# Kernel optimization log

Hardware: AMD Instinct MI355X
Metric: run time of the kernel (lower is better)

The kernel has to match this reference:

```python
import jax, jax.numpy as jnp
import numpy as np

B, L, D = 2, 1024, 512          # batch, seq_len, d_model
H, DK, DV, P = 8, 64, 64, 4     # heads, d_k, d_v, num masks
TEMP = DK ** 0.5
EPS = 1e-6


def setup_inputs() -> dict:
    key = jax.random.key(0)
    ks = jax.random.split(key, 11)
    s = 0.04  # ~xavier scale for these fan sizes
    q = jax.random.normal(ks[0], (B, L, D), jnp.float32)
    k = jax.random.normal(ks[1], (B, L, D), jnp.float32)
    v = jax.random.normal(ks[2], (B, L, D), jnp.float32)
    mask = (jax.random.uniform(ks[3], (P, 1, 1, L, L)) > 0.2).astype(jnp.float32)
    w_q = jax.random.normal(ks[4], (H * DK, D), jnp.float32) * s
    w_k = jax.random.normal(ks[5], (H * DK, D), jnp.float32) * s
    w_v = jax.random.normal(ks[6], (H * DV, D), jnp.float32) * s
    fc_w = jax.random.normal(ks[7], (D, H * DV), jnp.float32) * s
    fc_b = jnp.zeros((D,), jnp.float32)
    ln_g = jnp.ones((D,), jnp.float32)
    ln_b = jnp.zeros((D,), jnp.float32)
    return {"q": q, "k": k, "v": v, "mask": mask, "w_q": w_q, "w_k": w_k,
            "w_v": w_v, "fc_w": fc_w, "fc_b": fc_b, "ln_g": ln_g, "ln_b": ln_b}


def reference(q, k, v, mask, w_q, w_k, w_v, fc_w, fc_b, ln_g, ln_b):
    b, lq = q.shape[0], q.shape[1]
    lk = k.shape[1]
    residual = q
    # pre-LayerNorm on q (normalize_before=True)
    mu = jnp.mean(q, axis=-1, keepdims=True)
    var = jnp.mean(jnp.square(q - mu), axis=-1, keepdims=True)
    qn = (q - mu) * jax.lax.rsqrt(var + EPS) * ln_g + ln_b
    # projections -> [B,H,L,dk/dv]
    qh = jnp.einsum('bld,ed->ble', qn, w_q).reshape(b, lq, H, DK).transpose(0, 2, 1, 3)
    kh = jnp.einsum('bld,ed->ble', k, w_k).reshape(b, lk, H, DK).transpose(0, 2, 1, 3)
    vh = jnp.einsum('bld,ed->ble', v, w_v).reshape(b, lk, H, DV).transpose(0, 2, 1, 3)
    # shared scores, computed once: [B,H,Lq,Lk]
    attn = jnp.einsum('bhqd,bhkd->bhqk', qh / TEMP, kh)
    # per-mask additive bias, vectorized over P (dropout is identity in eval)
    ext = (1.0 - mask) * -10000.0                      # [P,1,1,Lq,Lk]
    probs = jax.nn.softmax(attn[None] + ext, axis=-1)  # [P,B,H,Lq,Lk]
    out = jnp.einsum('pbhqk,bhkd->pbhqd', probs, vh)   # [P,B,H,Lq,DV]
    out = out.transpose(0, 1, 3, 2, 4).reshape(P, b, lq, H * DV)
    out = jnp.einsum('pble,de->pbld', out, fc_w) + fc_b
    out = out + residual[None]
    return (out, attn)
```

## Files before the change

kernel.cpp:

```cpp
#include <hip/hip_runtime.h>
#include <math.h>

namespace {

constexpr int B = 2, L = 1024, D = 512, H = 8, DK = 64, DV = 64, P = 4;
constexpr float EPS = 1e-6f;
constexpr float ESHIFT = 16.0f;

typedef float f32x4 __attribute__((ext_vector_type(4)));
typedef short s16x8 __attribute__((ext_vector_type(8)));

__device__ inline unsigned short f2bf(float x) {
  union { float f; unsigned u; } v; v.f = x;
  unsigned r = v.u + 0x7fffu + ((v.u >> 16) & 1u);
  return (unsigned short)(r >> 16);
}

struct Cvt6 {
  const float* s[6];
  unsigned short* d[6];
  int cum[7];
};
constexpr int LNB = B * L;
constexpr int CVB = 3072;
constexpr int MKB = 512;

__global__ __launch_bounds__(256) void prep_kernel(
    const float* __restrict__ x, const float* __restrict__ g,
    const float* __restrict__ bta, unsigned short* __restrict__ y, Cvt6 a,
    const float* __restrict__ mask, unsigned* __restrict__ mpk) {
  int bid = blockIdx.x, t = threadIdx.x;
  if (bid < LNB) {
    const float* xr = x + (size_t)bid * D;
    unsigned short* yr = y + (size_t)bid * D;
    float v0 = xr[t], v1 = xr[t + 256];
    float s = v0 + v1;
#pragma unroll
    for (int off = 32; off; off >>= 1) s += __shfl_down(s, off, 64);
    __shared__ float red[4];
    if ((t & 63) == 0) red[t >> 6] = s;
    __syncthreads();
    float mu = (red[0] + red[1] + red[2] + red[3]) * (1.0f / D);
    float d0 = v0 - mu, d1 = v1 - mu;
    float vs = d0 * d0 + d1 * d1;
#pragma unroll
    for (int off = 32; off; off >>= 1) vs += __shfl_down(vs, off, 64);
    __syncthreads();
    if ((t & 63) == 0) red[t >> 6] = vs;
    __syncthreads();
    float var = (red[0] + red[1] + red[2] + red[3]) * (1.0f / D);
    float rstd = rsqrtf(var + EPS);
    yr[t] = f2bf(d0 * rstd * g[t] + bta[t]);
    yr[t + 256] = f2bf(d1 * rstd * g[t + 256] + bta[t + 256]);
  } else if (bid < LNB + CVB) {
    int e4 = ((bid - LNB) * 256 + t) * 4;
    int ti = 0;
    while (e4 >= a.cum[ti + 1]) ++ti;
    int off = e4 - a.cum[ti];
    float4 v = *(const float4*)(a.s[ti] + off);
    ushort4 o;
    o.x = f2bf(v.x); o.y = f2bf(v.y); o.z = f2bf(v.z); o.w = f2bf(v.w);
    *(ushort4*)(a.d[ti] + off) = o;
  } else {
    int gid = (bid - LNB - CVB) * 256 + t;
    const float4* src = (const float4*)mask + (size_t)gid * 8;
    unsigned bits = 0;
#pragma unroll
    for (int j = 0; j < 8; ++j) {
      float4 vv = src[j];
      bits |= (vv.x != 0.0f ? 1u : 0u) << (j * 4);
      bits |= (vv.y != 0.0f ? 2u : 0u) << (j * 4);
      bits |= (vv.z != 0.0f ? 4u : 0u) << (j * 4);
      bits |= (vv.w != 0.0f ? 8u : 0u) << (j * 4);
    }
    mpk[gid] = bits;
  }
}

template <bool BF16OUT, bool VTOUT>
__global__ __launch_bounds__(256) void bgemm_nt(
    const unsigned short* __restrict__ A, int lda, long sA0, long sA1,
    const unsigned short* __restrict__ Bm, int ldb, long sB0, long sB1,
    void* __restrict__ Cv, int ldc, long sC0, long sC1,
    int Z0, int K, float alpha,
    const float* __restrict__ bias, const float* __restrict__ resid, int rm,
    unsigned short* __restrict__ vtout) {
  int z = blockIdx.z;
  int z0 = z % Z0, z1 = z / Z0;
  A += (size_t)z0 * sA0 + (size_t)z1 * sA1;
  Bm += (size_t)z0 * sB0 + (size_t)z1 * sB1;
  size_t cOff = (size_t)z0 * sC0 + (size_t)z1 * sC1;
  int m0 = blockIdx.y * 128, n0 = blockIdx.x * 128;
  int t = threadIdx.x;
  int w = t >> 6, lane = t & 63, q4 = lane >> 4, ln16 = lane & 15;
  int wm = (w >> 1) * 64, wn = (w & 1) * 64;
  __shared__ __align__(16) unsigned short As[2][128][40];
  __shared__ __align__(16) unsigned short Bs[2][128][40];
  f32x4 acc[4][4];
#pragma unroll
  for (int i = 0; i < 4; ++i)
#pragma unroll
    for (int j = 0; j < 4; ++j)
#pragma unroll
      for (int r = 0; r < 4; ++r) acc[i][j][r] = 0.0f;
  int c0 = t, c1 = t + 256;
  const unsigned short* Ar0 = A + (size_t)(m0 + (c0 >> 2)) * lda + (c0 & 3) * 8;
  const unsigned short* Ar1 = A + (size_t)(m0 + (c1 >> 2)) * lda + (c1 & 3) * 8;
  const unsigned short* Br0 = Bm + (size_t)(n0 + (c0 >> 2)) * ldb + (c0 & 3) * 8;
  const unsigned short* Br1 = Bm + (size_t)(n0 + (c1 >> 2)) * ldb + (c1 & 3) * 8;
  {
    float4 a0 = *(const float4*)Ar0;
    float4 a1 = *(const float4*)Ar1;
    float4 b0 = *(const float4*)Br0;
    float4 b1 = *(const float4*)Br1;
    *(float4*)&As[0][c0 >> 2][(c0 & 3) * 8] = a0;
    *(float4*)&As[0][c1 >> 2][(c1 & 3) * 8] = a1;
    *(float4*)&Bs[0][c0 >> 2][(c0 & 3) * 8] = b0;
    *(float4*)&Bs[0][c1 >> 2][(c1 & 3) * 8] = b1;
  }
  int nIt = K >> 5;
  for (int it = 0; it < nIt; ++it) {
    int cur = it & 1;
    float4 na0, na1, nb0, nb1;
    if (it + 1 < nIt) {
      int kt = (it + 1) * 32;
      na0 = *(const float4*)(Ar0 + kt);
      na1 = *(const float4*)(Ar1 + kt);
      nb0 = *(const float4*)(Br0 + kt);
      nb1 = *(const float4*)(Br1 + kt);
    }
    __syncthreads();
    s16x8 af[4], bf[4];
#pragma unroll
    for (int mi = 0; mi < 4; ++mi)
      af[mi] = *(const s16x8*)&As[cur][wm + mi * 16 + ln16][q4 * 8];
#pragma unroll
    for (int ni = 0; ni < 4; ++ni)
      bf[ni] = *(const s16x8*)&Bs[cur][wn + ni * 16 + ln16][q4 * 8];
#pragma unroll
    for (int mi = 0; mi < 4; ++mi)
#pragma unroll
      for (int ni = 0; ni < 4; ++ni)
        acc[mi][ni] = __builtin_amdgcn_mfma_f32_16x16x32_bf16(
            af[mi], bf[ni], acc[mi][ni], 0, 0, 0);
    if (it + 1 < nIt) {
      int nb = 1 - cur;
      *(float4*)&As[nb][c0 >> 2][(c0 & 3) * 8] = na0;
      *(float4*)&As[nb][c1 >> 2][(c1 & 3) * 8] = na1;
      *(float4*)&Bs[nb][c0 >> 2][(c0 & 3) * 8] = nb0;
      *(float4*)&Bs[nb][c1 >> 2][(c1 & 3) * 8] = nb1;
    }
  }
  if (VTOUT && z0 == 2) {
#pragma unroll
    for (int mi = 0; mi < 4; ++mi)
#pragma unroll
      for (int ni = 0; ni < 4; ++ni) {
        int row0 = m0 + wm + mi * 16 + q4 * 4;
        int col = n0 + wn + ni * 16 + ln16;
        int bb = row0 >> 10, hh = col >> 6, dv = col & 63;
        ushort4 o;
        o.x = f2bf(acc[mi][ni][0]);
        o.y = f2bf(acc[mi][ni][1]);
        o.z = f2bf(acc[mi][ni][2]);
        o.w = f2bf(acc[mi][ni][3]);
        *(ushort4*)&vtout[((size_t)((bb * 8 + hh) * 64 + dv)) * 1024 +
                          (row0 & 1023)] = o;
      }
    return;
  }
#pragma unroll
  for (int mi = 0; mi < 4; ++mi)
#pragma unroll
    for (int r = 0; r < 4; ++r) {
      int row = m0 + wm + mi * 16 + q4 * 4 + r;
#pragma unroll
      for (int ni = 0; ni < 4; ++ni) {
        int col = n0 + wn + ni * 16 + ln16;
        float v = acc[mi][ni][r] * alpha;
        if (bias) v += bias[col];
        if (resid) v += resid[(size_t)(row & rm) * ldc + col];
        if (BF16OUT)
          ((unsigned short*)Cv)[cOff + (size_t)row * ldc + col] = f2bf(v);
        else
          ((float*)Cv)[cOff + (size_t)row * ldc + col] = v;
      }
    }
}

__global__ __launch_bounds__(256, 2) void fattn2_kernel(
    const unsigned short* __restrict__ qh,
    const unsigned short* __restrict__ khm, const unsigned* __restrict__ mpk,
    const unsigned short* __restrict__ vt, float* __restrict__ attn,
    unsigned short* __restrict__ outh) {
  int q0 = blockIdx.x * 32, bh = blockIdx.y;
  int b = bh >> 3, h = bh & 7;
  __shared__ __align__(16) unsigned short Es[3][32][72];
  __shared__ __align__(16) unsigned short Vs[2][64][72];
  __shared__ __align__(16) unsigned short Qs[32][72];
  __shared__ unsigned Mb[2][4][32][2];
  int t = threadIdx.x;
  int w = t >> 6, lane = t & 63, q4 = lane >> 4, ln16 = lane & 15;
  int vr = t >> 2, vk = (t & 3) * 16;
  int mp = t >> 6, mq = (t >> 1) & 31, md = t & 1;
  const unsigned short* vsrc = vt + ((size_t)bh * 64 + vr) * 1024 + vk;
  const unsigned* msrc = mpk + ((size_t)mp * L + q0 + mq) * 32 + md;
  const unsigned short* kbase = khm + (size_t)(b * L) * 512 + h * 64;
  float* arow = attn + (size_t)bh * L * L + (size_t)q0 * L;

  s16x8 ones;
#pragma unroll
  for (int j = 0; j < 8; ++j) ones[j] = (short)0x3F80;
  f32x4 acc[2][4], accs[2];
#pragma unroll
  for (int i = 0; i < 2; ++i) {
#pragma unroll
    for (int r = 0; r < 4; ++r) accs[i][r] = 0.0f;
#pragma unroll
    for (int j = 0; j < 4; ++j)
#pragma unroll
      for (int r = 0; r < 4; ++r) acc[i][j][r] = 0.0f;
  }
  s16x8 kreg[4][2];

#define KLOAD(dd)                                                              \
  do {                                                                         \
    const unsigned short* kb_ =                                                \
        kbase + (size_t)((dd) * 64 + ln16) * 512 + q4 * 8;                     \
    _Pragma("unroll") for (int ni = 0; ni < 4; ++ni)                           \
        _Pragma("unroll") for (int kk = 0; kk < 2; ++kk)                       \
            kreg[ni][kk] = *(const s16x8*)(kb_ + (size_t)ni * 16 * 512 +       \
                                           kk * 32);                           \
  } while (0)

#define QKCHUNK(dd)                                                            \
  do {                                                                         \
    f32x4 a2[2][4];                                                            \
    _Pragma("unroll") for (int mi = 0; mi < 2; ++mi)                           \
        _Pragma("unroll") for (int ni = 0; ni < 4; ++ni)                       \
            _Pragma("unroll") for (int r = 0; r < 4; ++r) a2[mi][ni][r] = 0.f; \
    _Pragma("unroll") for (int kk = 0; kk < 2; ++kk) {                         \
      s16x8 qf[2];                                                             \
      _Pragma("unroll") for (int mi = 0; mi < 2; ++mi) qf[mi] =                \
          *(const s16x8*)&Qs[mi * 16 + ln16][kk * 32 + q4 * 8];                \
      _Pragma("unroll") for (int mi = 0; mi < 2; ++mi)                         \
          _Pragma("unroll") for (int ni = 0; ni < 4; ++ni)                     \
              a2[mi][ni] = __builtin_amdgcn_mfma_f32_16x16x32_bf16(            \
                  qf[mi], kreg[ni][kk], a2[mi][ni], 0, 0, 0);                  \
    }                                                                          \
    int kc_ = (dd) * 64, eb_ = (dd) % 3;                                       \
    _Pragma("unroll") for (int mi = 0; mi < 2; ++mi)                           \
        _Pragma("unroll") for (int r = 0; r < 4; ++r) {                        \
      int row_ = mi * 16 + q4 * 4 + r;                                         \
      _Pragma("unroll") for (int ni = 0; ni < 4; ++ni) {                       \
        int col_ = ni * 16 + ln16;                                             \
        float v_ = a2[mi][ni][r] * 0.125f;                                     \
        arow[(size_t)row_ * L + kc_ + col_] = v_;                              \
        Es[eb_][row_][col_] = f2bf(__expf(v_ - ESHIFT));                       \
      }                                                                        \
    }                                                                          \
  } while (0)

  {
    int qr = t >> 3, qk = (t & 7) * 8;
    *(int4*)&Qs[qr][qk] =
        *(const int4*)(qh + (size_t)(b * L + q0 + qr) * 512 + h * 64 + qk);
  }
  *(int4*)&Vs[0][vr][vk] = *(const int4*)vsrc;
  *(int4*)&Vs[0][vr][vk + 8] = *(const int4*)(vsrc + 8);
  Mb[0][mp][mq][md] = msrc[0];
  KLOAD(w);
  __syncthreads();
  if (w == 0) QKCHUNK(0);
  else if (w == 1) QKCHUNK(1);
  __syncthreads();

  for (int c = 0; c < 16; ++c) {
    int4 nv0, nv1;
    unsigned nmb;
    if (c < 15) {
      const unsigned short* vs = vsrc + (c + 1) * 64;
      nv0 = *(const int4*)vs;
      nv1 = *(const int4*)(vs + 8);
      nmb = msrc[(c + 1) * 2];
    }
    if (c + 4 <= 15 && ((c + 4) & 3) == w) KLOAD(c + 4);
    {
      int b3 = c % 3, bv = c & 1;
      unsigned mby[2][2];
#pragma unroll
      for (int mi = 0; mi < 2; ++mi) {
        unsigned d0 = Mb[bv][w][mi * 16 + ln16][0];
        unsigned d1 = Mb[bv][w][mi * 16 + ln16][1];
        mby[mi][0] = (d0 >> (q4 * 8)) & 0xFFu;
        mby[mi][1] = (d1 >> (q4 * 8)) & 0xFFu;
      }
      s16x8 bfv[4][2];
#pragma unroll
      for (int ni = 0; ni < 4; ++ni)
#pragma unroll
        for (int kk = 0; kk < 2; ++kk)
          bfv[ni][kk] =
              *(const s16x8*)&Vs[bv][ni * 16 + ln16][kk * 32 + q4 * 8];
#pragma unroll
      for (int mi = 0; mi < 2; ++mi)
#pragma unroll
        for (int kk = 0; kk < 2; ++kk) {
          union { s16x8 s; unsigned u[4]; } ef;
          ef.s = *(const s16x8*)&Es[b3][mi * 16 + ln16][kk * 32 + q4 * 8];
          unsigned bb = mby[mi][kk];
#pragma unroll
          for (int dd = 0; dd < 4; ++dd) {
            unsigned mm = (((bb >> (2 * dd)) & 1u) ? 0xFFFFu : 0u) |
                          (((bb >> (2 * dd + 1)) & 1u) ? 0xFFFF0000u : 0u);
            ef.u[dd] &= mm;
          }
#pragma unroll
          for (int ni = 0; ni < 4; ++ni)
            acc[mi][ni] = __builtin_amdgcn_mfma_f32_16x16x32_bf16(
                ef.s, bfv[ni][kk], acc[mi][ni], 0, 0, 0);
          accs[mi] = __builtin_amdgcn_mfma_f32_16x16x32_bf16(ef.s, ones,
                                                             accs[mi], 0, 0, 0);
        }
    }
    if (c + 2 <= 15 && ((c + 2) & 3) == w) QKCHUNK(c + 2);
    if (c < 15) {
      int nb = (c + 1) & 1;
      *(int4*)&Vs[nb][vr][vk] = nv0;
      *(int4*)&Vs[nb][vr][vk + 8] = nv1;
      Mb[nb][mp][mq][md] = nmb;
    }
    __syncthreads();
  }
#undef KLOAD
#undef QKCHUNK

#pragma unroll
  for (int mi = 0; mi < 2; ++mi)
#pragma unroll
    for (int r = 0; r < 4; ++r) {
      int row = mi * 16 + q4 * 4 + r;
      float inv = 1.0f / accs[mi][r];
      size_t o = ((size_t)(w * B + b) * L + q0 + row) * 512 + h * 64 + ln16;
#pragma unroll
      for (int ni = 0; ni < 4; ++ni)
        outh[o + ni * 16] = f2bf(acc[mi][ni][r] * inv);
    }
}

}

extern "C" void kernel_launch(void* const* d_in, const int* in_sizes, int n_in,
                              void* d_out, int out_size, void* d_ws,
                              size_t ws_size, hipStream_t stream) {
  const float* q = (const float*)d_in[0];
  const float* k = (const float*)d_in[1];
  const float* v = (const float*)d_in[2];
  const float* mask = (const float*)d_in[3];
  const float* w_q = (const float*)d_in[4];
  const float* w_k = (const float*)d_in[5];
  const float* w_v = (const float*)d_in[6];
  const float* fc_w = (const float*)d_in[7];
  const float* fc_b = (const float*)d_in[8];
  const float* ln_g = (const float*)d_in[9];
  const float* ln_b = (const float*)d_in[10];

  float* out = (float*)d_out;
  float* attn = out + (size_t)P * B * L * D;

  unsigned short* wsu = (unsigned short*)d_ws;
  const size_t T1 = (size_t)B * L * D;
  const size_t TW = (size_t)D * D;
  unsigned short* qkv_bf = wsu;
  unsigned short* w_bf = qkv_bf + 3 * T1;
  unsigned short* fcw_bf = w_bf + 3 * TW;
  unsigned short* qh_bf = fcw_bf + TW;
  unsigned short* vt = qh_bf + 2 * T1;
  unsigned short* outh = vt + T1;
  unsigned* mpk = (unsigned*)(outh + 4 * T1);

  Cvt6 ca;
  ca.s[0] = k; ca.s[1] = v; ca.s[2] = w_q; ca.s[3] = w_k; ca.s[4] = w_v;
  ca.s[5] = fc_w;
  ca.d[0] = qkv_bf + T1; ca.d[1] = qkv_bf + 2 * T1;
  ca.d[2] = w_bf; ca.d[3] = w_bf + TW; ca.d[4] = w_bf + 2 * TW;
  ca.d[5] = fcw_bf;
  ca.cum[0] = 0;
  int sizes[6] = {(int)T1, (int)T1, (int)TW, (int)TW, (int)TW, (int)TW};
  for (int i = 0; i < 6; ++i) ca.cum[i + 1] = ca.cum[i] + sizes[i];
  prep_kernel<<<LNB + CVB + MKB, 256, 0, stream>>>(q, ln_g, ln_b, qkv_bf, ca,
                                                   mask, mpk);

  bgemm_nt<true, true><<<dim3(D / 128, (B * L) / 128, 3), 256, 0, stream>>>(
      qkv_bf, D, (long)T1, 0, w_bf, D, (long)TW, 0, qh_bf, D, (long)T1, 0,
      3, D, 1.0f, nullptr, nullptr, 0, vt);

  fattn2_kernel<<<dim3(L / 32, B * H), 256, 0, stream>>>(
      qh_bf, qh_bf + T1, mpk, vt, attn, outh);

  bgemm_nt<false, false><<<dim3(D / 128, (P * B * L) / 128, 1), 256, 0,
                           stream>>>(
      outh, D, 0, 0, fcw_bf, D, 0, 0, out, D, 0, 0, 1, D, 1.0f, fc_b, q,
      B * L - 1, nullptr);
}
```

Baseline: 198.8 us.

## Fuse fp32-to-bf16 conversion of k, v and weights into GEMM tile loads

Removes the separate conversion pass in the prep kernel that wrote bf16 copies of k, v and all four weight matrices. The GEMMs now read fp32 directly and convert to bf16 while staging tiles into shared memory. This avoids one extra round trip through global memory for those tensors. In exchange, the GEMMs load twice as many bytes per tile, and weights are reconverted by every block that reads them. Output stores for attn scores and the final result are also switched to nontemporal stores.

```diff
diff --git a/kernel.cpp b/kernel.cpp
--- a/kernel.cpp
+++ b/kernel.cpp
@@ -16,18 +16,21 @@
   return (unsigned short)(r >> 16);
 }
 
-struct Cvt6 {
-  const float* s[6];
-  unsigned short* d[6];
-  int cum[7];
-};
+__device__ inline s16x8 cvtf8(float4 a, float4 b) {
+  s16x8 r;
+  r[0] = (short)f2bf(a.x); r[1] = (short)f2bf(a.y);
+  r[2] = (short)f2bf(a.z); r[3] = (short)f2bf(a.w);
+  r[4] = (short)f2bf(b.x); r[5] = (short)f2bf(b.y);
+  r[6] = (short)f2bf(b.z); r[7] = (short)f2bf(b.w);
+  return r;
+}
+
 constexpr int LNB = B * L;
-constexpr int CVB = 3072;
 constexpr int MKB = 512;
 
 __global__ __launch_bounds__(256) void prep_kernel(
     const float* __restrict__ x, const float* __restrict__ g,
-    const float* __restrict__ bta, unsigned short* __restrict__ y, Cvt6 a,
+    const float* __restrict__ bta, unsigned short* __restrict__ y,
     const float* __restrict__ mask, unsigned* __restrict__ mpk) {
   int bid = blockIdx.x, t = threadIdx.x;
   if (bid < LNB) {
@@ -52,17 +55,8 @@
     float rstd = rsqrtf(var + EPS);
     yr[t] = f2bf(d0 * rstd * g[t] + bta[t]);
     yr[t + 256] = f2bf(d1 * rstd * g[t + 256] + bta[t + 256]);
-  } else if (bid < LNB + CVB) {
-    int e4 = ((bid - LNB) * 256 + t) * 4;
-    int ti = 0;
-    while (e4 >= a.cum[ti + 1]) ++ti;
-    int off = e4 - a.cum[ti];
-    float4 v = *(const float4*)(a.s[ti] + off);
-    ushort4 o;
-    o.x = f2bf(v.x); o.y = f2bf(v.y); o.z = f2bf(v.z); o.w = f2bf(v.w);
-    *(ushort4*)(a.d[ti] + off) = o;
   } else {
-    int gid = (bid - LNB - CVB) * 256 + t;
+    int gid = (bid - LNB) * 256 + t;
     const float4* src = (const float4*)mask + (size_t)gid * 8;
     unsigned bits = 0;
 #pragma unroll
@@ -77,19 +71,17 @@
   }
 }
 
-template <bool BF16OUT, bool VTOUT>
-__global__ __launch_bounds__(256) void bgemm_nt(
-    const unsigned short* __restrict__ A, int lda, long sA0, long sA1,
-    const unsigned short* __restrict__ Bm, int ldb, long sB0, long sB1,
-    void* __restrict__ Cv, int ldc, long sC0, long sC1,
-    int Z0, int K, float alpha,
-    const float* __restrict__ bias, const float* __restrict__ resid, int rm,
-    unsigned short* __restrict__ vtout) {
-  int z = blockIdx.z;
-  int z0 = z % Z0, z1 = z / Z0;
-  A += (size_t)z0 * sA0 + (size_t)z1 * sA1;
-  Bm += (size_t)z0 * sB0 + (size_t)z1 * sB1;
-  size_t cOff = (size_t)z0 * sC0 + (size_t)z1 * sC1;
+template <bool PROJ>
+__global__ __launch_bounds__(256) void bgemm2(
+    const unsigned short* __restrict__ Abf, const float* __restrict__ Af1,
+    const float* __restrict__ Af2, const float* __restrict__ Bf0,
+    const float* __restrict__ Bf1, const float* __restrict__ Bf2,
+    unsigned short* __restrict__ Cbf, unsigned short* __restrict__ vtout,
+    float* __restrict__ Cf, const float* __restrict__ bias,
+    const float* __restrict__ resid) {
+  int z0 = PROJ ? blockIdx.z : 0;
+  const float* Afp = (PROJ && z0) ? (z0 == 1 ? Af1 : Af2) : nullptr;
+  const float* Bfp = PROJ ? (z0 == 0 ? Bf0 : (z0 == 1 ? Bf1 : Bf2)) : Bf0;
   int m0 = blockIdx.y * 128, n0 = blockIdx.x * 128;
   int t = threadIdx.x;
   int w = t >> 6, lane = t & 63, q4 = lane >> 4, ln16 = lane & 15;
@@ -104,30 +96,49 @@
 #pragma unroll
       for (int r = 0; r < 4; ++r) acc[i][j][r] = 0.0f;
   int c0 = t, c1 = t + 256;
-  const unsigned short* Ar0 = A + (size_t)(m0 + (c0 >> 2)) * lda + (c0 & 3) * 8;
-  const unsigned short* Ar1 = A + (size_t)(m0 + (c1 >> 2)) * lda + (c1 & 3) * 8;
-  const unsigned short* Br0 = Bm + (size_t)(n0 + (c0 >> 2)) * ldb + (c0 & 3) * 8;
-  const unsigned short* Br1 = Bm + (size_t)(n0 + (c1 >> 2)) * ldb + (c1 & 3) * 8;
+  size_t eA0 = (size_t)(m0 + (c0 >> 2)) * 512 + (c0 & 3) * 8;
+  size_t eA1 = (size_t)(m0 + (c1 >> 2)) * 512 + (c1 & 3) * 8;
+  size_t eB0 = (size_t)(n0 + (c0 >> 2)) * 512 + (c0 & 3) * 8;
+  size_t eB1 = (size_t)(n0 + (c1 >> 2)) * 512 + (c1 & 3) * 8;
   {
-    float4 a0 = *(const float4*)Ar0;
-    float4 a1 = *(const float4*)Ar1;
-    float4 b0 = *(const float4*)Br0;
-    float4 b1 = *(const float4*)Br1;
-    *(float4*)&As[0][c0 >> 2][(c0 & 3) * 8] = a0;
-    *(float4*)&As[0][c1 >> 2][(c1 & 3) * 8] = a1;
-    *(float4*)&Bs[0][c0 >> 2][(c0 & 3) * 8] = b0;
-    *(float4*)&Bs[0][c1 >> 2][(c1 & 3) * 8] = b1;
-  }
-  int nIt = K >> 5;
+    s16x8 wa0, wa1;
+    if (Afp) {
+      wa0 = cvtf8(*(const float4*)(Afp + eA0), *(const float4*)(Afp + eA0 + 4));
+      wa1 = cvtf8(*(const float4*)(Afp + eA1), *(const float4*)(Afp + eA1 + 4));
+    } else {
+      wa0 = *(const s16x8*)(Abf + eA0);
+      wa1 = *(const s16x8*)(Abf + eA1);
+    }
+    s16x8 wb0 =
+        cvtf8(*(const float4*)(Bfp + eB0), *(const float4*)(Bfp + eB0 + 4));
+    s16x8 wb1 =
+        cvtf8(*(const float4*)(Bfp + eB1), *(const float4*)(Bfp + eB1 + 4));
+    *(s16x8*)&As[0][c0 >> 2][(c0 & 3) * 8] = wa0;
+    *(s16x8*)&As[0][c1 >> 2][(c1 & 3) * 8] = wa1;
+    *(s16x8*)&Bs[0][c0 >> 2][(c0 & 3) * 8] = wb0;
+    *(s16x8*)&Bs[0][c1 >> 2][(c1 & 3) * 8] = wb1;
+  }
+  constexpr int nIt = 512 >> 5;
   for (int it = 0; it < nIt; ++it) {
     int cur = it & 1;
-    float4 na0, na1, nb0, nb1;
+    s16x8 nab0, nab1;
+    float4 naf0[2], naf1[2];
+    float4 nbf0[2], nbf1[2];
     if (it + 1 < nIt) {
       int kt = (it + 1) * 32;
-      na0 = *(const float4*)(Ar0 + kt);
-      na1 = *(const float4*)(Ar1 + kt);
-      nb0 = *(const float4*)(Br0 + kt);
-      nb1 = *(const float4*)(Br1 + kt);
+      if (Afp) {
+        naf0[0] = *(const float4*)(Afp + eA0 + kt);
+        naf0[1] = *(const float4*)(Afp + eA0 + kt + 4);
+        naf1[0] = *(const float4*)(Afp + eA1 + kt);
+        naf1[1] = *(const float4*)(Afp + eA1 + kt + 4);
+      } else {
+        nab0 = *(const s16x8*)(Abf + eA0 + kt);
+        nab1 = *(const s16x8*)(Abf + eA1 + kt);
+      }
+      nbf0[0] = *(const float4*)(Bfp + eB0 + kt);
+      nbf0[1] = *(const float4*)(Bfp + eB0 + kt + 4);
+      nbf1[0] = *(const float4*)(Bfp + eB1 + kt);
+      nbf1[1] = *(const float4*)(Bfp + eB1 + kt + 4);
     }
     __syncthreads();
     s16x8 af[4], bf[4];
@@ -145,13 +156,15 @@
             af[mi], bf[ni], acc[mi][ni], 0, 0, 0);
     if (it + 1 < nIt) {
       int nb = 1 - cur;
-      *(float4*)&As[nb][c0 >> 2][(c0 & 3) * 8] = na0;
-      *(float4*)&As[nb][c1 >> 2][(c1 & 3) * 8] = na1;
-      *(float4*)&Bs[nb][c0 >> 2][(c0 & 3) * 8] = nb0;
-      *(float4*)&Bs[nb][c1 >> 2][(c1 & 3) * 8] = nb1;
-    }
-  }
-  if (VTOUT && z0 == 2) {
+      s16x8 wa0 = Afp ? cvtf8(naf0[0], naf0[1]) : nab0;
+      s16x8 wa1 = Afp ? cvtf8(naf1[0], naf1[1]) : nab1;
+      *(s16x8*)&As[nb][c0 >> 2][(c0 & 3) * 8] = wa0;
+      *(s16x8*)&As[nb][c1 >> 2][(c1 & 3) * 8] = wa1;
+      *(s16x8*)&Bs[nb][c0 >> 2][(c0 & 3) * 8] = cvtf8(nbf0[0], nbf0[1]);
+      *(s16x8*)&Bs[nb][c1 >> 2][(c1 & 3) * 8] = cvtf8(nbf1[0], nbf1[1]);
+    }
+  }
+  if (PROJ && z0 == 2) {
 #pragma unroll
     for (int mi = 0; mi < 4; ++mi)
 #pragma unroll
@@ -169,23 +182,34 @@
       }
     return;
   }
-#pragma unroll
-  for (int mi = 0; mi < 4; ++mi)
-#pragma unroll
-    for (int r = 0; r < 4; ++r) {
-      int row = m0 + wm + mi * 16 + q4 * 4 + r;
-#pragma unroll
-      for (int ni = 0; ni < 4; ++ni) {
-        int col = n0 + wn + ni * 16 + ln16;
-        float v = acc[mi][ni][r] * alpha;
-        if (bias) v += bias[col];
-        if (resid) v += resid[(size_t)(row & rm) * ldc + col];
-        if (BF16OUT)
-          ((unsigned short*)Cv)[cOff + (size_t)row * ldc + col] = f2bf(v);
-        else
-          ((float*)Cv)[cOff + (size_t)row * ldc + col] = v;
+  if (PROJ) {
+    unsigned short* Cp = Cbf + (size_t)z0 * ((size_t)B * L * D);
+#pragma unroll
+    for (int mi = 0; mi < 4; ++mi)
+#pragma unroll
+      for (int r = 0; r < 4; ++r) {
+        int row = m0 + wm + mi * 16 + q4 * 4 + r;
+#pragma unroll
+        for (int ni = 0; ni < 4; ++ni) {
+          int col = n0 + wn + ni * 16 + ln16;
+          Cp[(size_t)row * 512 + col] = f2bf(acc[mi][ni][r]);
+        }
       }
-    }
+  } else {
+#pragma unroll
+    for (int mi = 0; mi < 4; ++mi)
+#pragma unroll
+      for (int r = 0; r < 4; ++r) {
+        int row = m0 + wm + mi * 16 + q4 * 4 + r;
+#pragma unroll
+        for (int ni = 0; ni < 4; ++ni) {
+          int col = n0 + wn + ni * 16 + ln16;
+          float vv = acc[mi][ni][r] + bias[col] +
+                     resid[(size_t)(row & (B * L - 1)) * 512 + col];
+          __builtin_nontemporal_store(vv, &Cf[(size_t)row * 512 + col]);
+        }
+      }
+  }
 }
 
 __global__ __launch_bounds__(256, 2) void fattn2_kernel(
@@ -255,7 +279,7 @@
       _Pragma("unroll") for (int ni = 0; ni < 4; ++ni) {                       \
         int col_ = ni * 16 + ln16;                                             \
         float v_ = a2[mi][ni][r] * 0.125f;                                     \
-        arow[(size_t)row_ * L + kc_ + col_] = v_;                              \
+        __builtin_nontemporal_store(v_, &arow[(size_t)row_ * L + kc_ + col_]); \
         Es[eb_][row_][col_] = f2bf(__expf(v_ - ESHIFT));                       \
       }                                                                        \
     }                                                                          \
@@ -370,36 +394,21 @@
 
   unsigned short* wsu = (unsigned short*)d_ws;
   const size_t T1 = (size_t)B * L * D;
-  const size_t TW = (size_t)D * D;
-  unsigned short* qkv_bf = wsu;
-  unsigned short* w_bf = qkv_bf + 3 * T1;
-  unsigned short* fcw_bf = w_bf + 3 * TW;
-  unsigned short* qh_bf = fcw_bf + TW;
+  unsigned short* qbf = wsu;
+  unsigned short* qh_bf = qbf + T1;
   unsigned short* vt = qh_bf + 2 * T1;
   unsigned short* outh = vt + T1;
   unsigned* mpk = (unsigned*)(outh + 4 * T1);
 
-  Cvt6 ca;
-  ca.s[0] = k; ca.s[1] = v; ca.s[2] = w_q; ca.s[3] = w_k; ca.s[4] = w_v;
-  ca.s[5] = fc_w;
-  ca.d[0] = qkv_bf + T1; ca.d[1] = qkv_bf + 2 * T1;
-  ca.d[2] = w_bf; ca.d[3] = w_bf + TW; ca.d[4] = w_bf + 2 * TW;
-  ca.d[5] = fcw_bf;
-  ca.cum[0] = 0;
-  int sizes[6] = {(int)T1, (int)T1, (int)TW, (int)TW, (int)TW, (int)TW};
-  for (int i = 0; i < 6; ++i) ca.cum[i + 1] = ca.cum[i] + sizes[i];
-  prep_kernel<<<LNB + CVB + MKB, 256, 0, stream>>>(q, ln_g, ln_b, qkv_bf, ca,
-                                                   mask, mpk);
-
-  bgemm_nt<true, true><<<dim3(D / 128, (B * L) / 128, 3), 256, 0, stream>>>(
-      qkv_bf, D, (long)T1, 0, w_bf, D, (long)TW, 0, qh_bf, D, (long)T1, 0,
-      3, D, 1.0f, nullptr, nullptr, 0, vt);
+  prep_kernel<<<LNB + MKB, 256, 0, stream>>>(q, ln_g, ln_b, qbf, mask, mpk);
+
+  bgemm2<true><<<dim3(D / 128, (B * L) / 128, 3), 256, 0, stream>>>(
+      qbf, k, v, w_q, w_k, w_v, qh_bf, vt, nullptr, nullptr, nullptr);
 
   fattn2_kernel<<<dim3(L / 32, B * H), 256, 0, stream>>>(
       qh_bf, qh_bf + T1, mpk, vt, attn, outh);
 
-  bgemm_nt<false, false><<<dim3(D / 128, (P * B * L) / 128, 1), 256, 0,
-                           stream>>>(
-      outh, D, 0, 0, fcw_bf, D, 0, 0, out, D, 0, 0, 1, D, 1.0f, fc_b, q,
-      B * L - 1, nullptr);
-}
+  bgemm2<false><<<dim3(D / 128, (P * B * L) / 128, 1), 256, 0, stream>>>(
+      outh, nullptr, nullptr, fc_w, nullptr, nullptr, nullptr, nullptr, out,
+      fc_b, q);
+}
```

New measurement: 190.1 us. -4.4%, faster.
